# Optimization experiments

Measured on AMD Instinct MI355X. Metric: run time of the kernel, lower is better.

## Reference

```python
import jax, jax.numpy as jnp
import numpy as np

B, T, D, H = 4, 2048, 1024, 16
HD = D // H  # head_dim = 64


def setup_inputs() -> dict:
    key = jax.random.key(0)
    k1, k2, k3, k4, k5 = jax.random.split(key, 5)
    scale = 1.0 / np.sqrt(D)
    return {
        "x": jax.random.normal(k1, (B, T, D), dtype=jnp.float32),
        "mask": jnp.ones((B, T), dtype=jnp.int32),
        "W_qkv": jax.random.normal(k2, (D, 3 * D), dtype=jnp.float32) * scale,
        "b_qkv": jax.random.normal(k3, (3 * D,), dtype=jnp.float32) * 0.01,
        "W_out": jax.random.normal(k4, (D, D), dtype=jnp.float32) * scale,
        "b_out": jax.random.normal(k5, (D,), dtype=jnp.float32) * 0.01,
    }


def reference(x, mask, W_qkv, b_qkv, W_out, b_out):
    Bx, Tx, Dm = x.shape
    qkv = x @ W_qkv + b_qkv                      # [B,T,3D]
    qkv = qkv.reshape(Bx, Tx, 3, H, HD)
    qkv = jnp.transpose(qkv, (2, 0, 3, 1, 4))    # [3,B,H,T,hd]
    q, k, v = qkv[0], qkv[1], qkv[2]
    att = jnp.einsum("bhqd,bhkd->bhqk", q, k) / jnp.sqrt(jnp.float32(HD))
    m = (mask[:, None, None, :] == 0)            # [B,1,1,T]
    att = jnp.where(m, jnp.float32(-1e9), att)
    att = jax.nn.softmax(att, axis=-1)
    out = jnp.einsum("bhqk,bhkd->bhqd", att, v)  # [B,H,T,hd]
    out = jnp.transpose(out, (0, 2, 1, 3)).reshape(Bx, Tx, Dm)
    return out @ W_out + b_out
```

## Files before the change

kernel.cpp:

```cpp
#include <hip/hip_runtime.h>
#include <hip/hip_bf16.h>
#include <stdint.h>

#define B_  4
#define T_  2048
#define D_  1024
#define H_  16
#define HD_ 64

typedef short s16x8 __attribute__((ext_vector_type(8)));
typedef short s16x4 __attribute__((ext_vector_type(4)));
typedef float f32x4 __attribute__((ext_vector_type(4)));

#define MFMA32(a, b, c) __builtin_amdgcn_mfma_f32_16x16x32_bf16(a, b, c, 0, 0, 0)

#if __has_builtin(__builtin_amdgcn_exp2f)
#define FEXP2(x) __builtin_amdgcn_exp2f(x)
#else
#define FEXP2(x) exp2f(x)
#endif

__device__ __forceinline__ unsigned short f2bf(float f) {
    union { float f; unsigned int u; } v; v.f = f;
    unsigned int r = v.u + 0x7fffu + ((v.u >> 16) & 1u);
    return (unsigned short)(r >> 16);
}

__device__ __forceinline__ unsigned int pkbf(float a, float b) {
    __hip_bfloat162 h = __float22bfloat162_rn(float2{a, b});
    union { __hip_bfloat162 h; unsigned int u; } v; v.h = h;
    return v.u;
}

__device__ __forceinline__ void async16(const void* g, void* l) {
    __builtin_amdgcn_global_load_lds(
        (const __attribute__((address_space(1))) unsigned int*)g,
        (__attribute__((address_space(3))) unsigned int*)l, 16, 0, 0);
}

__global__ __launch_bounds__(256)
void prep_kernel(const float* __restrict__ x, unsigned short* __restrict__ xb,
                 const float* __restrict__ Wq, unsigned short* __restrict__ Wqt,
                 const float* __restrict__ Wo, unsigned short* __restrict__ Wot) {
    const int blk = blockIdx.x;
    const int tid = threadIdx.x;
    if (blk < 8192) {
        const int i = blk * 256 + tid;
        float4 v = ((const float4*)x)[i];
        ushort4 o;
        o.x = f2bf(v.x); o.y = f2bf(v.y); o.z = f2bf(v.z); o.w = f2bf(v.w);
        ((ushort4*)xb)[i] = o;
        return;
    }
    __shared__ float t[32][33];
    const float* W; unsigned short* Wt; int K, N, bx, by;
    if (blk < 11264) {
        const int idx = blk - 8192;
        W = Wq; Wt = Wqt; K = 1024; N = 3072;
        bx = (idx % 96) * 32; by = (idx / 96) * 32;
    } else {
        const int idx = blk - 11264;
        W = Wo; Wt = Wot; K = 1024; N = 1024;
        bx = (idx % 32) * 32; by = (idx / 32) * 32;
    }
    const int tx = tid & 31, ty = tid >> 5;
    #pragma unroll
    for (int j = 0; j < 32; j += 8)
        t[ty + j][tx] = W[(size_t)(by + ty + j) * N + bx + tx];
    __syncthreads();
    #pragma unroll
    for (int j = 0; j < 32; j += 8)
        Wt[(size_t)(bx + ty + j) * K + by + tx] = f2bf(t[tx][ty + j]);
}

template <int MODE>
__global__ __launch_bounds__(256)
void gemm_bt_kernel(const unsigned short* __restrict__ A,
                    const unsigned short* __restrict__ Bt,
                    const float* __restrict__ bias,
                    float* __restrict__ Cf,
                    unsigned short* __restrict__ Qo,
                    unsigned short* __restrict__ Ko,
                    unsigned short* __restrict__ Vo,
                    int M, int N, int K) {
    __shared__ __align__(16) unsigned short SMEM[2 * 128 * 64];
    unsigned short* As = SMEM;
    unsigned short* Bs = SMEM + 128 * 64;
    const int tid = threadIdx.x;
    const int w = tid >> 6, lane = tid & 63;
    const int laneN = lane & 15, quad = lane >> 4;
    const int rm0 = blockIdx.x * 128;
    const int rn0 = blockIdx.y * 128;
    const int wr = (w >> 1) * 64, wc = (w & 1) * 64;

    f32x4 acc[4][4] = {};

    for (int kk = 0; kk < K; kk += 64) {
        #pragma unroll
        for (int i = 0; i < 4; ++i) {
            const int c = i * 256 + tid;
            const int row = c >> 3, s = c & 7, g = s ^ (row & 7);
            async16(A + (size_t)(rm0 + row) * K + kk + g * 8,
                    (char*)As + (size_t)c * 16);
        }
        #pragma unroll
        for (int i = 0; i < 4; ++i) {
            const int c = i * 256 + tid;
            const int row = c >> 3, s = c & 7, g = s ^ (row & 7);
            async16(Bt + (size_t)(rn0 + row) * K + kk + g * 8,
                    (char*)Bs + (size_t)c * 16);
        }
        __syncthreads();
        s16x8 av[2][4], bv[2][4];
        #pragma unroll
        for (int h = 0; h < 2; ++h) {
            #pragma unroll
            for (int ms = 0; ms < 4; ++ms) {
                const int row = wr + ms * 16 + laneN;
                av[h][ms] = *(const s16x8*)&As[row * 64 + ((h * 4 + quad) ^ (row & 7)) * 8];
            }
            #pragma unroll
            for (int ns = 0; ns < 4; ++ns) {
                const int row = wc + ns * 16 + laneN;
                bv[h][ns] = *(const s16x8*)&Bs[row * 64 + ((h * 4 + quad) ^ (row & 7)) * 8];
            }
        }
        #pragma unroll
        for (int ms = 0; ms < 4; ++ms)
            #pragma unroll
            for (int ns = 0; ns < 4; ++ns) {
                acc[ms][ns] = MFMA32(av[0][ms], bv[0][ns], acc[ms][ns]);
                acc[ms][ns] = MFMA32(av[1][ms], bv[1][ns], acc[ms][ns]);
            }
        __syncthreads();
    }

    if (MODE == 0) {
        #pragma unroll
        for (int ms = 0; ms < 4; ++ms) {
            const int gm0 = rm0 + wr + ms * 16 + quad * 4;
            #pragma unroll
            for (int ns = 0; ns < 4; ++ns) {
                const int gn = rn0 + wc + ns * 16 + laneN;
                const float bb = bias[gn];
                #pragma unroll
                for (int r = 0; r < 4; ++r)
                    Cf[(size_t)(gm0 + r) * N + gn] = acc[ms][ns][r] + bb;
            }
        }
    } else {
        const int s = rn0 >> 10;
        const int bidx = rm0 >> 11, t0 = rm0 & (T_ - 1);
        if (s < 2) {
            const float fs = (s == 0) ? 0.125f * 1.44269504088896f : 1.0f;
            unsigned short* P = (s == 0) ? Qo : Ko;
            #pragma unroll
            for (int ms = 0; ms < 4; ++ms) {
                const int lm0 = wr + ms * 16 + quad * 4;
                #pragma unroll
                for (int ns = 0; ns < 4; ++ns) {
                    const int gn = rn0 + wc + ns * 16 + laneN;
                    const float bb = bias[gn];
                    const int rr = gn & 1023, hh = rr >> 6, dd = rr & 63;
                    const size_t base = ((size_t)(bidx * H_ + hh) * T_ + t0);
                    #pragma unroll
                    for (int r = 0; r < 4; ++r)
                        P[(base + lm0 + r) * HD_ + dd] =
                            f2bf((acc[ms][ns][r] + bb) * fs);
                }
            }
        } else {
            #pragma unroll
            for (int ms = 0; ms < 4; ++ms) {
                const int lm0 = wr + ms * 16 + quad * 4;
                #pragma unroll
                for (int ns = 0; ns < 4; ++ns) {
                    const int nl = wc + ns * 16 + laneN;
                    const float bb = bias[rn0 + nl];
                    const int sw = (nl & 7) << 3;
                    #pragma unroll
                    for (int r = 0; r < 4; ++r)
                        SMEM[nl * 128 + ((lm0 + r) ^ sw)] =
                            f2bf(acc[ms][ns][r] + bb);
                }
            }
            __syncthreads();
            const int nl = tid >> 1, half = tid & 1;
            const int hh = nl >> 6, d = nl & 63;
            const int hAbs = bidx * H_ + ((rn0 & 1023) >> 6) + hh;
            unsigned short* rowp = Vo + ((size_t)hAbs * HD_ + d) * T_ + t0;
            const int swz = nl & 7;
            #pragma unroll
            for (int j = 0; j < 8; ++j) {
                const s16x8 vv = *(const s16x8*)&SMEM[nl * 128 + half * 64 + j * 8];
                const int mlog = half * 64 + ((j ^ swz) * 8);
                *(s16x8*)(rowp + mlog) = vv;
            }
        }
    }
}

__global__ __launch_bounds__(512, 4)
void attn_kernel(const unsigned short* __restrict__ Q,
                 const unsigned short* __restrict__ Kb,
                 const unsigned short* __restrict__ VT,
                 const int* __restrict__ mask,
                 unsigned short* __restrict__ Out) {
    __shared__ __align__(16) unsigned short Ks[2][128 * 64];
    __shared__ __align__(16) unsigned short Vs[2][64 * 128];
    __shared__ float biasF[T_];
    const int tid = threadIdx.x;
    const int lane = tid & 63;
    const int laneN = lane & 15, quad = lane >> 4;
    const int x7 = laneN & 7;
    const int bh = blockIdx.x;
    const int b = bh >> 4, h = bh & 15;
    const int qbase = blockIdx.y * 256 + (tid >> 6) * 32;

    for (int i = tid; i < T_; i += 512)
        biasF[i] = mask[b * T_ + i] ? 0.f : -1.0e9f;

    s16x8 qf[2][2];
    #pragma unroll
    for (int qg = 0; qg < 2; ++qg) {
        const size_t qoff = ((size_t)bh * T_ + qbase + qg * 16 + laneN) * HD_ + quad * 8;
        qf[qg][0] = *(const s16x8*)&Q[qoff];
        qf[qg][1] = *(const s16x8*)&Q[qoff + 32];
    }

    s16x8 ones;
    #pragma unroll
    for (int j = 0; j < 8; ++j) ones[j] = (short)0x3F80;

    const size_t kRow0 = (size_t)bh * T_ * HD_;
    const size_t vRow0 = (size_t)bh * HD_ * T_;

    auto issueTile = [&](int kt, int bufsel) {
        const int kbase = kt * 128;
        #pragma unroll
        for (int i = 0; i < 2; ++i) {
            const int c = i * 512 + tid;
            const int row = c >> 3, s = c & 7;
            const int fk = (row & 3) | (((row >> 3) & 1) << 2);
            const int g = s ^ fk;
            async16(Kb + kRow0 + (size_t)(kbase + row) * HD_ + g * 8,
                    &Ks[bufsel][c * 8]);
        }
        #pragma unroll
        for (int i = 0; i < 2; ++i) {
            const int c = i * 512 + tid;
            const int d = c >> 4, s = c & 15, g = s ^ (d & 15);
            async16(VT + vRow0 + (size_t)d * T_ + kbase + g * 8,
                    &Vs[bufsel][c * 8]);
        }
    };

    issueTile(0, 0);

    f32x4 O[2][4] = {};
    f32x4 liacc[2] = {};

    const int rowA = ((laneN >> 2) << 3) + (laneN & 3);

    #pragma unroll 2
    for (int kt = 0; kt < T_ / 128; ++kt) {
        const int buf = kt & 1;
        const int kbase = kt * 128;
        __syncthreads();
        if (kt + 1 < T_ / 128) issueTile(kt + 1, buf ^ 1);

        #pragma unroll
        for (int g32 = 0; g32 < 4; ++g32) {
            const int ra = g32 * 32 + rowA;
            const s16x8 kA0 = *(const s16x8*)&Ks[buf][(ra * 8 + (quad ^ x7)) * 8];
            const s16x8 kA1 = *(const s16x8*)&Ks[buf][(ra * 8 + ((4 + quad) ^ x7)) * 8];
            const s16x8 kB0 = *(const s16x8*)&Ks[buf][((ra + 4) * 8 + (quad ^ x7)) * 8];
            const s16x8 kB1 = *(const s16x8*)&Ks[buf][((ra + 4) * 8 + ((4 + quad) ^ x7)) * 8];
            const f32x4 bA = *(const f32x4*)&biasF[kbase + g32 * 32 + quad * 8];
            const f32x4 bB = *(const f32x4*)&biasF[kbase + g32 * 32 + quad * 8 + 4];
            s16x8 pf[2];
            #pragma unroll
            for (int qg = 0; qg < 2; ++qg) {
                f32x4 Sa = bA, Sb = bB;
                Sa = MFMA32(kA0, qf[qg][0], Sa);
                Sa = MFMA32(kA1, qf[qg][1], Sa);
                Sb = MFMA32(kB0, qf[qg][0], Sb);
                Sb = MFMA32(kB1, qf[qg][1], Sb);
                #pragma unroll
                for (int r = 0; r < 4; ++r) {
                    Sa[r] = FEXP2(Sa[r]);
                    Sb[r] = FEXP2(Sb[r]);
                }
                union { s16x8 v; unsigned int u[4]; } pu;
                pu.u[0] = pkbf(Sa[0], Sa[1]);
                pu.u[1] = pkbf(Sa[2], Sa[3]);
                pu.u[2] = pkbf(Sb[0], Sb[1]);
                pu.u[3] = pkbf(Sb[2], Sb[3]);
                pf[qg] = pu.v;
            }
            s16x8 vf[4];
            #pragma unroll
            for (int nt = 0; nt < 4; ++nt) {
                const int d = nt * 16 + laneN;
                const int slog = g32 * 4 + quad;
                vf[nt] = *(const s16x8*)&Vs[buf][(d * 16 + (slog ^ (d & 15))) * 8];
            }
            #pragma unroll
            for (int qg = 0; qg < 2; ++qg) {
                #pragma unroll
                for (int nt = 0; nt < 4; ++nt)
                    O[qg][nt] = MFMA32(pf[qg], vf[nt], O[qg][nt]);
                liacc[qg] = MFMA32(pf[qg], ones, liacc[qg]);
            }
        }
    }

    #pragma unroll
    for (int qg = 0; qg < 2; ++qg) {
        #pragma unroll
        for (int r = 0; r < 4; ++r) {
            const float inv = 1.0f / liacc[qg][r];
            const int tq = qbase + qg * 16 + quad * 4 + r;
            #pragma unroll
            for (int nt = 0; nt < 4; ++nt)
                Out[(size_t)(b * T_ + tq) * D_ + h * HD_ + nt * 16 + laneN] =
                    f2bf(O[qg][nt][r] * inv);
        }
    }
}

extern "C" void kernel_launch(void* const* d_in, const int* in_sizes, int n_in,
                              void* d_out, int out_size, void* d_ws, size_t ws_size,
                              hipStream_t stream) {
    const float* x     = (const float*)d_in[0];
    const int*   mask  = (const int*)d_in[1];
    const float* W_qkv = (const float*)d_in[2];
    const float* b_qkv = (const float*)d_in[3];
    const float* W_out = (const float*)d_in[4];
    const float* b_out = (const float*)d_in[5];
    float* out = (float*)d_out;

    unsigned short* ws = (unsigned short*)d_ws;
    const size_t NX = (size_t)B_ * T_ * D_;
    unsigned short* xb  = ws;
    unsigned short* Qb  = xb + NX;
    unsigned short* Kb  = Qb + NX;
    unsigned short* Vtb = Kb + NX;
    unsigned short* Wqt = Vtb + NX;
    unsigned short* Wot = Wqt + (size_t)3 * D_ * D_;
    unsigned short* attn = xb;

    prep_kernel<<<12288, 256, 0, stream>>>(x, xb, W_qkv, Wqt, W_out, Wot);
    gemm_bt_kernel<1><<<dim3(B_ * T_ / 128, 3 * D_ / 128), 256, 0, stream>>>(
        xb, Wqt, b_qkv, nullptr, Qb, Kb, Vtb, B_ * T_, 3 * D_, D_);
    attn_kernel<<<dim3(B_ * H_, T_ / 256), 512, 0, stream>>>(Qb, Kb, Vtb, mask, attn);
    gemm_bt_kernel<0><<<dim3(B_ * T_ / 128, D_ / 128), 256, 0, stream>>>(
        attn, Wot, b_out, out, nullptr, nullptr, nullptr, B_ * T_, D_, D_);
}
```

Measured before the change: 271.2 us.

## Double-buffer GEMM K-loop and shrink attention KV tiles to 64

The GEMM now double-buffers its A/B shared-memory tiles. It issues the next K-slab's async loads after reading the current fragments, which removes one barrier per iteration and overlaps loads with MFMA. The attention kernel halves its K/V tile from 128 to 64 keys, cutting shared memory per block, and splits the QK/exp phase from the PV phase within each tile. The tradeoff is GEMM shared memory doubling to 64KB, which may lower occupancy, and twice as many barriers per attention block.

```diff
diff --git a/kernel.cpp b/kernel.cpp
--- a/kernel.cpp
+++ b/kernel.cpp
@@ -83,9 +83,7 @@
                     unsigned short* __restrict__ Ko,
                     unsigned short* __restrict__ Vo,
                     int M, int N, int K) {
-    __shared__ __align__(16) unsigned short SMEM[2 * 128 * 64];
-    unsigned short* As = SMEM;
-    unsigned short* Bs = SMEM + 128 * 64;
+    __shared__ __align__(16) unsigned short SMEM[4 * 128 * 64];
     const int tid = threadIdx.x;
     const int w = tid >> 6, lane = tid & 63;
     const int laneN = lane & 15, quad = lane >> 4;
@@ -95,7 +93,9 @@
 
     f32x4 acc[4][4] = {};
 
-    for (int kk = 0; kk < K; kk += 64) {
+    auto issueG = [&](int kk, int bufsel) {
+        unsigned short* As = SMEM + bufsel * 8192;
+        unsigned short* Bs = SMEM + 16384 + bufsel * 8192;
         #pragma unroll
         for (int i = 0; i < 4; ++i) {
             const int c = i * 256 + tid;
@@ -110,7 +110,15 @@
             async16(Bt + (size_t)(rn0 + row) * K + kk + g * 8,
                     (char*)Bs + (size_t)c * 16);
         }
+    };
+
+    issueG(0, 0);
+    const int KI = K >> 6;
+    for (int it = 0; it < KI; ++it) {
+        const int buf = it & 1;
         __syncthreads();
+        const unsigned short* As = SMEM + buf * 8192;
+        const unsigned short* Bs = SMEM + 16384 + buf * 8192;
         s16x8 av[2][4], bv[2][4];
         #pragma unroll
         for (int h = 0; h < 2; ++h) {
@@ -125,6 +133,7 @@
                 bv[h][ns] = *(const s16x8*)&Bs[row * 64 + ((h * 4 + quad) ^ (row & 7)) * 8];
             }
         }
+        if (it + 1 < KI) issueG((it + 1) << 6, buf ^ 1);
         #pragma unroll
         for (int ms = 0; ms < 4; ++ms)
             #pragma unroll
@@ -132,7 +141,6 @@
                 acc[ms][ns] = MFMA32(av[0][ms], bv[0][ns], acc[ms][ns]);
                 acc[ms][ns] = MFMA32(av[1][ms], bv[1][ns], acc[ms][ns]);
             }
-        __syncthreads();
     }
 
     if (MODE == 0) {
@@ -170,6 +178,7 @@
                 }
             }
         } else {
+            __syncthreads();
             #pragma unroll
             for (int ms = 0; ms < 4; ++ms) {
                 const int lm0 = wr + ms * 16 + quad * 4;
@@ -206,16 +215,17 @@
                  const unsigned short* __restrict__ VT,
                  const int* __restrict__ mask,
                  unsigned short* __restrict__ Out) {
-    __shared__ __align__(16) unsigned short Ks[2][128 * 64];
-    __shared__ __align__(16) unsigned short Vs[2][64 * 128];
+    __shared__ __align__(16) unsigned short Ks[2][64 * 64];
+    __shared__ __align__(16) unsigned short Vs[2][64 * 64];
     __shared__ float biasF[T_];
     const int tid = threadIdx.x;
     const int lane = tid & 63;
+    const int w = tid >> 6;
     const int laneN = lane & 15, quad = lane >> 4;
     const int x7 = laneN & 7;
     const int bh = blockIdx.x;
     const int b = bh >> 4, h = bh & 15;
-    const int qbase = blockIdx.y * 256 + (tid >> 6) * 32;
+    const int qbase = blockIdx.y * 256 + w * 32;
 
     for (int i = tid; i < T_; i += 512)
         biasF[i] = mask[b * T_ + i] ? 0.f : -1.0e9f;
@@ -236,20 +246,18 @@
     const size_t vRow0 = (size_t)bh * HD_ * T_;
 
     auto issueTile = [&](int kt, int bufsel) {
-        const int kbase = kt * 128;
-        #pragma unroll
-        for (int i = 0; i < 2; ++i) {
-            const int c = i * 512 + tid;
+        const int kbase = kt * 64;
+        {
+            const int c = tid;
             const int row = c >> 3, s = c & 7;
             const int fk = (row & 3) | (((row >> 3) & 1) << 2);
             const int g = s ^ fk;
             async16(Kb + kRow0 + (size_t)(kbase + row) * HD_ + g * 8,
                     &Ks[bufsel][c * 8]);
         }
-        #pragma unroll
-        for (int i = 0; i < 2; ++i) {
-            const int c = i * 512 + tid;
-            const int d = c >> 4, s = c & 15, g = s ^ (d & 15);
+        {
+            const int c = tid;
+            const int d = c >> 3, s = c & 7, g = s ^ (d & 7);
             async16(VT + vRow0 + (size_t)d * T_ + kbase + g * 8,
                     &Vs[bufsel][c * 8]);
         }
@@ -263,14 +271,15 @@
     const int rowA = ((laneN >> 2) << 3) + (laneN & 3);
 
     #pragma unroll 2
-    for (int kt = 0; kt < T_ / 128; ++kt) {
+    for (int kt = 0; kt < T_ / 64; ++kt) {
         const int buf = kt & 1;
-        const int kbase = kt * 128;
+        const int kbase = kt * 64;
         __syncthreads();
-        if (kt + 1 < T_ / 128) issueTile(kt + 1, buf ^ 1);
-
-        #pragma unroll
-        for (int g32 = 0; g32 < 4; ++g32) {
+        if (kt + 1 < T_ / 64) issueTile(kt + 1, buf ^ 1);
+
+        s16x8 pf[2][2];
+        #pragma unroll
+        for (int g32 = 0; g32 < 2; ++g32) {
             const int ra = g32 * 32 + rowA;
             const s16x8 kA0 = *(const s16x8*)&Ks[buf][(ra * 8 + (quad ^ x7)) * 8];
             const s16x8 kA1 = *(const s16x8*)&Ks[buf][(ra * 8 + ((4 + quad) ^ x7)) * 8];
@@ -278,7 +287,6 @@
             const s16x8 kB1 = *(const s16x8*)&Ks[buf][((ra + 4) * 8 + ((4 + quad) ^ x7)) * 8];
             const f32x4 bA = *(const f32x4*)&biasF[kbase + g32 * 32 + quad * 8];
             const f32x4 bB = *(const f32x4*)&biasF[kbase + g32 * 32 + quad * 8 + 4];
-            s16x8 pf[2];
             #pragma unroll
             for (int qg = 0; qg < 2; ++qg) {
                 f32x4 Sa = bA, Sb = bB;
@@ -296,21 +304,24 @@
                 pu.u[1] = pkbf(Sa[2], Sa[3]);
                 pu.u[2] = pkbf(Sb[0], Sb[1]);
                 pu.u[3] = pkbf(Sb[2], Sb[3]);
-                pf[qg] = pu.v;
-            }
+                pf[qg][g32] = pu.v;
+            }
+        }
+
+        #pragma unroll
+        for (int g32 = 0; g32 < 2; ++g32) {
             s16x8 vf[4];
             #pragma unroll
             for (int nt = 0; nt < 4; ++nt) {
                 const int d = nt * 16 + laneN;
-                const int slog = g32 * 4 + quad;
-                vf[nt] = *(const s16x8*)&Vs[buf][(d * 16 + (slog ^ (d & 15))) * 8];
+                vf[nt] = *(const s16x8*)&Vs[buf][(d * 8 + ((g32 * 4 + quad) ^ x7)) * 8];
             }
             #pragma unroll
             for (int qg = 0; qg < 2; ++qg) {
                 #pragma unroll
                 for (int nt = 0; nt < 4; ++nt)
-                    O[qg][nt] = MFMA32(pf[qg], vf[nt], O[qg][nt]);
-                liacc[qg] = MFMA32(pf[qg], ones, liacc[qg]);
+                    O[qg][nt] = MFMA32(pf[qg][g32], vf[nt], O[qg][nt]);
+                liacc[qg] = MFMA32(pf[qg][g32], ones, liacc[qg]);
             }
         }
     }
```

Result: faster. 257.5 us (-5.0%).
